# Kernel optimization log

Hardware: AMD Instinct MI355X
Metric: run time of the kernel (lower is better)

## Reference

```python
import jax, jax.numpy as jnp
import numpy as np

B, T, U = 8192, 1024, 1024  # batch, token_length, units

def _glorot(key, shape):
    fan_in, fan_out = shape
    limit = np.sqrt(6.0 / (fan_in + fan_out))
    return jax.random.uniform(key, shape, jnp.float32, -limit, limit)

def setup_inputs() -> dict:
    key = jax.random.key(0)
    ks = jax.random.split(key, 7)
    x = jax.random.normal(ks[0], (B, T), jnp.float32)
    h = jax.random.normal(ks[1], (B, U), jnp.float32)
    c = jax.random.normal(ks[2], (B, U), jnp.float32)
    W_i = _glorot(ks[3], (T + U, U))
    W_f = _glorot(ks[4], (T + U, U))
    W_g = _glorot(ks[5], (T + U, U))
    W_o = _glorot(ks[6], (T + U, U))
    b_i = jnp.zeros((U,), jnp.float32)
    b_f = jnp.zeros((U,), jnp.float32)
    b_g = jnp.zeros((U,), jnp.float32)
    b_o = jnp.zeros((U,), jnp.float32)
    return {"x": x, "h": h, "c": c, "W_i": W_i, "W_f": W_f, "W_g": W_g,
            "W_o": W_o, "b_i": b_i, "b_f": b_f, "b_g": b_g, "b_o": b_o}

def reference(x, h, c, W_i, W_f, W_g, W_o, b_i, b_f, b_g, b_o):
    x_h = jnp.concatenate([x, h], axis=-1)  # [B, T+U]
    # fused wide GEMM over the four gates
    W = jnp.concatenate([W_i, W_f, W_g, W_o], axis=1)  # [T+U, 4U]
    b = jnp.concatenate([b_i, b_f, b_g, b_o], axis=0)  # [4U]
    z = x_h @ W + b  # [B, 4U]
    zi, zf, zg, zo = jnp.split(z, 4, axis=-1)
    i = jax.nn.sigmoid(zi)
    f = jax.nn.sigmoid(zf)
    g = jnp.tanh(zg)
    o = jax.nn.sigmoid(zo)
    c_new = f * c + i * g
    h_new = o * jnp.tanh(c_new)
    return (h_new, c_new)
```

## Files before the change

### kernel.cpp

```cpp
#include <hip/hip_runtime.h>
#include <hip/hip_bf16.h>
#include <stdint.h>


typedef float f32x4 __attribute__((ext_vector_type(4)));
typedef __bf16 bf16x8 __attribute__((ext_vector_type(8)));

static __device__ __forceinline__ void gll16(const void* g, void* l) {
  __builtin_amdgcn_global_load_lds(
      (const __attribute__((address_space(1))) void*)g,
      (__attribute__((address_space(3))) void*)l, 16, 0, 0);
}

static __device__ __forceinline__ unsigned short f2bf(float f) {
  union { __hip_bfloat16 h; unsigned short u; } v{__float2bfloat16(f)};
  return v.u;
}

__global__ void pack_a(const float* __restrict__ x, const float* __restrict__ h,
                       char* __restrict__ Ap) {
  int row = blockIdx.x;
  int c8  = threadIdx.x;
  int kt  = c8 >> 2, kq = c8 & 3;
  int gk  = c8 * 8;
  const float* src = (gk < 1024) ? (x + (size_t)row * 1024 + gk)
                                 : (h + (size_t)row * 1024 + (gk - 1024));
  float4 lo = *(const float4*)src;
  float4 hi = *(const float4*)(src + 4);
  __attribute__((aligned(16))) unsigned short o[8] = {
      f2bf(lo.x), f2bf(lo.y), f2bf(lo.z), f2bf(lo.w),
      f2bf(hi.x), f2bf(hi.y), f2bf(hi.z), f2bf(hi.w) };
  int r = row & 255;
  int chunk = r * 4 + (kq ^ ((r >> 1) & 3));
  char* dst = Ap + ((size_t)((row >> 8) * 64 + kt)) * 16384 + chunk * 16;
  *(int4*)dst = *(const int4*)o;
}

__global__ void pack_w(const float* __restrict__ Wi, const float* __restrict__ Wf,
                       const float* __restrict__ Wg, const float* __restrict__ Wo,
                       char* __restrict__ Wp) {
  __shared__ float tile[32][65];
  int kt = blockIdx.x;
  int cbo = blockIdx.y;
  int g = blockIdx.z;
  const float* W = (g == 0) ? Wi : (g == 1) ? Wf : (g == 2) ? Wg : Wo;
  int t = threadIdx.x;
  {
    int k  = t >> 3;
    int c8 = (t & 7) * 8;
    const float* s = W + (size_t)(kt * 32 + k) * 1024 + cbo * 64 + c8;
    float4 lo = *(const float4*)s;
    float4 hi = *(const float4*)(s + 4);
    tile[k][c8 + 0] = lo.x; tile[k][c8 + 1] = lo.y; tile[k][c8 + 2] = lo.z; tile[k][c8 + 3] = lo.w;
    tile[k][c8 + 4] = hi.x; tile[k][c8 + 5] = hi.y; tile[k][c8 + 6] = hi.z; tile[k][c8 + 7] = hi.w;
  }
  __syncthreads();
  {
    int cl = t >> 2;
    int kq = t & 3;
    __attribute__((aligned(16))) unsigned short o[8];
#pragma unroll
    for (int j = 0; j < 8; ++j) o[j] = f2bf(tile[kq * 8 + j][cl]);
    int gc = ((cl >> 4) & 3) * 64 + g * 16 + (cl & 15);
    int chunk = gc * 4 + (kq ^ ((gc >> 1) & 3));
    char* dst = Wp + ((size_t)(cbo * 64 + kt)) * 16384 + chunk * 16;
    *(int4*)dst = *(const int4*)o;
  }
}

__global__ __launch_bounds__(512, 2)
void lstm_gemm(const char* __restrict__ Ap, const char* __restrict__ Wp,
               const float* __restrict__ c_in,
               const float* __restrict__ b_i, const float* __restrict__ b_f,
               const float* __restrict__ b_g, const float* __restrict__ b_o,
               float* __restrict__ out) {
  __shared__ __align__(128) char smem[131072];

  int tid = threadIdx.x;
  int w = tid >> 6, lane = tid & 63, l15 = lane & 15, lq = lane >> 4;
  int wm = w >> 2, wc = w & 3;

  int bid = blockIdx.x;
  int wg = (bid & 7) * 64 + (bid >> 3);
  int rbB = wg >> 4, cb = wg & 15;

  const char* aT = Ap + (size_t)rbB * (64 * 16384);
  const char* bT = Wp + (size_t)cb * (64 * 16384);

  f32x4 acc[8][4] = {};

  int aOff[8], bOff[4];
#pragma unroll
  for (int m = 0; m < 8; ++m) {
    int r = wm * 128 + m * 16 + l15;
    aOff[m] = r * 64 + ((lq ^ ((r >> 1) & 3)) << 4);
  }
#pragma unroll
  for (int n = 0; n < 4; ++n) {
    int gc = wc * 64 + n * 16 + l15;
    bOff[n] = gc * 64 + ((lq ^ ((gc >> 1) & 3)) << 4);
  }

  auto stgA = [&](int kt) {
    const char* s = aT + (size_t)kt * 16384 + tid * 16;
    char* d = smem + (kt & 3) * 32768 + tid * 16;
    gll16(s, d); gll16(s + 8192, d + 8192);
  };
  auto stgB = [&](int kt) {
    const char* s = bT + (size_t)kt * 16384 + tid * 16;
    char* d = smem + (kt & 3) * 32768 + 16384 + tid * 16;
    gll16(s, d); gll16(s + 8192, d + 8192);
  };

  stgA(0); stgB(0); stgA(1); stgB(1); stgA(2); stgB(2);
  asm volatile("s_waitcnt vmcnt(8)" ::: "memory");
  __builtin_amdgcn_s_barrier();

  for (int j = 0; j < 64; ++j) {
    const char* sA = smem + (j & 3) * 32768;
    const char* sB = sA + 16384;
    int js = (j + 3) & 63;

    bf16x8 aF[4], bF[4], aG[4];
#pragma unroll
    for (int m = 0; m < 4; ++m) aF[m] = *(const bf16x8*)(sA + aOff[m]);
#pragma unroll
    for (int n = 0; n < 4; ++n) bF[n] = *(const bf16x8*)(sB + bOff[n]);
    stgA(js);
    __builtin_amdgcn_s_barrier();
    __builtin_amdgcn_s_setprio(1);
#pragma unroll
    for (int m = 0; m < 4; ++m)
#pragma unroll
      for (int n = 0; n < 4; ++n)
        acc[m][n] = __builtin_amdgcn_mfma_f32_16x16x32_bf16(aF[m], bF[n], acc[m][n], 0, 0, 0);
    __builtin_amdgcn_s_setprio(0);
    __builtin_amdgcn_s_barrier();

#pragma unroll
    for (int m = 0; m < 4; ++m) aG[m] = *(const bf16x8*)(sA + aOff[4 + m]);
    stgB(js);
    __builtin_amdgcn_s_barrier();
    __builtin_amdgcn_s_setprio(1);
#pragma unroll
    for (int m = 0; m < 4; ++m)
#pragma unroll
      for (int n = 0; n < 4; ++n)
        acc[4 + m][n] = __builtin_amdgcn_mfma_f32_16x16x32_bf16(aG[m], bF[n], acc[4 + m][n], 0, 0, 0);
    __builtin_amdgcn_s_setprio(0);
    asm volatile("s_waitcnt vmcnt(8)" ::: "memory");
    __builtin_amdgcn_s_barrier();
  }

  int col = (cb * 4 + wc) * 16 + l15;
  float Bi = b_i[col], Bf = b_f[col], Bg = b_g[col], Bo = b_o[col];
  const size_t HN = (size_t)8192 * 1024;
#pragma unroll
  for (int mf = 0; mf < 8; ++mf) {
    int row0 = rbB * 256 + wm * 128 + mf * 16 + lq * 4;
#pragma unroll
    for (int r = 0; r < 4; ++r) {
      int row = row0 + r;
      float xi = acc[mf][0][r] + Bi, xf = acc[mf][1][r] + Bf;
      float xg = acc[mf][2][r] + Bg, xo = acc[mf][3][r] + Bo;
      float iv = 1.f / (1.f + __expf(-xi));
      float fv = 1.f / (1.f + __expf(-xf));
      float gv = 1.f - 2.f / (__expf(2.f * xg) + 1.f);
      float ov = 1.f / (1.f + __expf(-xo));
      float cv = c_in[(size_t)row * 1024 + col];
      float cn = fv * cv + iv * gv;
      float tc = 1.f - 2.f / (__expf(2.f * cn) + 1.f);
      out[(size_t)row * 1024 + col]      = ov * tc;
      out[HN + (size_t)row * 1024 + col] = cn;
    }
  }
}

extern "C" void kernel_launch(void* const* d_in, const int* in_sizes, int n_in,
                              void* d_out, int out_size, void* d_ws, size_t ws_size,
                              hipStream_t stream) {
  const float* x  = (const float*)d_in[0];
  const float* h  = (const float*)d_in[1];
  const float* c  = (const float*)d_in[2];
  const float* Wi = (const float*)d_in[3];
  const float* Wf = (const float*)d_in[4];
  const float* Wg = (const float*)d_in[5];
  const float* Wo = (const float*)d_in[6];
  const float* bi = (const float*)d_in[7];
  const float* bf = (const float*)d_in[8];
  const float* bg = (const float*)d_in[9];
  const float* bo = (const float*)d_in[10];

  char* Ap = (char*)d_ws;
  char* Wp = Ap + (size_t)8192 * 2048 * 2;
  float* out = (float*)d_out;

  hipLaunchKernelGGL(pack_a, dim3(8192), dim3(256), 0, stream, x, h, Ap);
  hipLaunchKernelGGL(pack_w, dim3(64, 16, 4), dim3(256), 0, stream, Wi, Wf, Wg, Wo, Wp);
  hipLaunchKernelGGL(lstm_gemm, dim3(512), dim3(512), 0, stream,
                     Ap, Wp, c, bi, bf, bg, bo, out);
}
```

Before: 313.3 us.

## Use K=64 tiles with double-buffered LDS and four-quadrant MFMA pipeline

Repacks A and W into 64-wide K tiles split into 128-row halves with an 8-way XOR swizzle. The GEMM main loop moves from 64 steps with 32-wide K and a 4-stage ring to 32 steps with 64-wide K and 2 LDS buffers. Each step is split into four MFMA quadrants interleaved with partial LDS reads and staggered global-to-LDS loads. The goal is fewer barriers per unit of work and finer overlap of loads with MFMA, at the cost of shallower prefetch and more complex wait accounting.

```diff
diff --git a/kernel.cpp b/kernel.cpp
--- a/kernel.cpp
+++ b/kernel.cpp
@@ -21,7 +21,7 @@
                        char* __restrict__ Ap) {
   int row = blockIdx.x;
   int c8  = threadIdx.x;
-  int kt  = c8 >> 2, kq = c8 & 3;
+  int kt  = c8 >> 3, q = c8 & 7;
   int gk  = c8 * 8;
   const float* src = (gk < 1024) ? (x + (size_t)row * 1024 + gk)
                                  : (h + (size_t)row * 1024 + (gk - 1024));
@@ -30,41 +30,48 @@
   __attribute__((aligned(16))) unsigned short o[8] = {
       f2bf(lo.x), f2bf(lo.y), f2bf(lo.z), f2bf(lo.w),
       f2bf(hi.x), f2bf(hi.y), f2bf(hi.z), f2bf(hi.w) };
-  int r = row & 255;
-  int chunk = r * 4 + (kq ^ ((r >> 1) & 3));
-  char* dst = Ap + ((size_t)((row >> 8) * 64 + kt)) * 16384 + chunk * 16;
-  *(int4*)dst = *(const int4*)o;
+  int rbB = row >> 8, half = (row >> 7) & 1, r = row & 127;
+  size_t dst = (((size_t)rbB * 32 + kt) * 2 + half) * 16384
+             + (size_t)(r * 8 + (q ^ (r & 7))) * 16;
+  *(int4*)(Ap + dst) = *(const int4*)o;
 }
 
 __global__ void pack_w(const float* __restrict__ Wi, const float* __restrict__ Wf,
                        const float* __restrict__ Wg, const float* __restrict__ Wo,
                        char* __restrict__ Wp) {
-  __shared__ float tile[32][65];
+  __shared__ float tile[64][65];
   int kt = blockIdx.x;
-  int cbo = blockIdx.y;
-  int g = blockIdx.z;
+  int cb = blockIdx.y;
+  int g  = blockIdx.z;
   const float* W = (g == 0) ? Wi : (g == 1) ? Wf : (g == 2) ? Wg : Wo;
   int t = threadIdx.x;
   {
-    int k  = t >> 3;
-    int c8 = (t & 7) * 8;
-    const float* s = W + (size_t)(kt * 32 + k) * 1024 + cbo * 64 + c8;
-    float4 lo = *(const float4*)s;
-    float4 hi = *(const float4*)(s + 4);
-    tile[k][c8 + 0] = lo.x; tile[k][c8 + 1] = lo.y; tile[k][c8 + 2] = lo.z; tile[k][c8 + 3] = lo.w;
-    tile[k][c8 + 4] = hi.x; tile[k][c8 + 5] = hi.y; tile[k][c8 + 6] = hi.z; tile[k][c8 + 7] = hi.w;
+    int k  = t >> 2;
+    int c8 = (t & 3) * 16;
+    const float* s = W + (size_t)(kt * 64 + k) * 1024 + cb * 64 + c8;
+#pragma unroll
+    for (int j4 = 0; j4 < 4; ++j4) {
+      float4 v = *(const float4*)(s + j4 * 4);
+      tile[k][c8 + j4 * 4 + 0] = v.x; tile[k][c8 + j4 * 4 + 1] = v.y;
+      tile[k][c8 + j4 * 4 + 2] = v.z; tile[k][c8 + j4 * 4 + 3] = v.w;
+    }
   }
   __syncthreads();
   {
     int cl = t >> 2;
     int kq = t & 3;
-    __attribute__((aligned(16))) unsigned short o[8];
-#pragma unroll
-    for (int j = 0; j < 8; ++j) o[j] = f2bf(tile[kq * 8 + j][cl]);
-    int gc = ((cl >> 4) & 3) * 64 + g * 16 + (cl & 15);
-    int chunk = gc * 4 + (kq ^ ((gc >> 1) & 3));
-    char* dst = Wp + ((size_t)(cbo * 64 + kt)) * 16384 + chunk * 16;
-    *(int4*)dst = *(const int4*)o;
+    int rloc = (cl >> 4) * 64 + g * 16 + (cl & 15);
+    int half = rloc >> 7, r = rloc & 127;
+#pragma unroll
+    for (int p = 0; p < 2; ++p) {
+      int q = kq + p * 4;
+      __attribute__((aligned(16))) unsigned short o[8];
+#pragma unroll
+      for (int j = 0; j < 8; ++j) o[j] = f2bf(tile[q * 8 + j][cl]);
+      size_t dst = (((size_t)cb * 32 + kt) * 2 + half) * 16384
+                 + (size_t)(r * 8 + (q ^ (r & 7))) * 16;
+      *(int4*)(Wp + dst) = *(const int4*)o;
+    }
   }
 }
 
@@ -84,73 +91,111 @@
   int wg = (bid & 7) * 64 + (bid >> 3);
   int rbB = wg >> 4, cb = wg & 15;
 
-  const char* aT = Ap + (size_t)rbB * (64 * 16384);
-  const char* bT = Wp + (size_t)cb * (64 * 16384);
+  const char* aT = Ap + (size_t)rbB * (32 * 2 * 16384);
+  const char* bT = Wp + (size_t)cb  * (32 * 2 * 16384);
 
   f32x4 acc[8][4] = {};
 
-  int aOff[8], bOff[4];
-#pragma unroll
-  for (int m = 0; m < 8; ++m) {
-    int r = wm * 128 + m * 16 + l15;
-    aOff[m] = r * 64 + ((lq ^ ((r >> 1) & 3)) << 4);
-  }
-#pragma unroll
-  for (int n = 0; n < 4; ++n) {
-    int gc = wc * 64 + n * 16 + l15;
-    bOff[n] = gc * 64 + ((lq ^ ((gc >> 1) & 3)) << 4);
-  }
-
-  auto stgA = [&](int kt) {
-    const char* s = aT + (size_t)kt * 16384 + tid * 16;
-    char* d = smem + (kt & 3) * 32768 + tid * 16;
-    gll16(s, d); gll16(s + 8192, d + 8192);
-  };
-  auto stgB = [&](int kt) {
-    const char* s = bT + (size_t)kt * 16384 + tid * 16;
-    char* d = smem + (kt & 3) * 32768 + 16384 + tid * 16;
-    gll16(s, d); gll16(s + 8192, d + 8192);
-  };
-
-  stgA(0); stgB(0); stgA(1); stgB(1); stgA(2); stgB(2);
-  asm volatile("s_waitcnt vmcnt(8)" ::: "memory");
-  __builtin_amdgcn_s_barrier();
-
-  for (int j = 0; j < 64; ++j) {
-    const char* sA = smem + (j & 3) * 32768;
-    const char* sB = sA + 16384;
-    int js = (j + 3) & 63;
-
-    bf16x8 aF[4], bF[4], aG[4];
-#pragma unroll
-    for (int m = 0; m < 4; ++m) aF[m] = *(const bf16x8*)(sA + aOff[m]);
-#pragma unroll
-    for (int n = 0; n < 4; ++n) bF[n] = *(const bf16x8*)(sB + bOff[n]);
-    stgA(js);
-    __builtin_amdgcn_s_barrier();
-    __builtin_amdgcn_s_setprio(1);
+  unsigned aOff[8][2], bOff[4][2];
+#pragma unroll
+  for (int mf = 0; mf < 8; ++mf) {
+    int r = mf * 16 + l15;
+#pragma unroll
+    for (int ks = 0; ks < 2; ++ks) {
+      int q = ks * 4 + lq;
+      aOff[mf][ks] = (unsigned)(wm * 16384 + (r * 8 + (q ^ (r & 7))) * 16);
+    }
+  }
+#pragma unroll
+  for (int nf = 0; nf < 4; ++nf) {
+    int r = (wc & 1) * 64 + nf * 16 + l15;
+#pragma unroll
+    for (int ks = 0; ks < 2; ++ks) {
+      int q = ks * 4 + lq;
+      bOff[nf][ks] = (unsigned)(32768 + (wc >> 1) * 16384 + (r * 8 + (q ^ (r & 7))) * 16);
+    }
+  }
+
+  auto stA = [&](int kt, int h) {
+    size_t s = (((size_t)(kt & 31)) * 2 + h) * 16384 + (size_t)tid * 16;
+    char* d = smem + (kt & 1) * 65536 + h * 16384 + tid * 16;
+    gll16(aT + s, d); gll16(aT + s + 8192, d + 8192);
+  };
+  auto stB = [&](int kt, int h) {
+    size_t s = (((size_t)(kt & 31)) * 2 + h) * 16384 + (size_t)tid * 16;
+    char* d = smem + (kt & 1) * 65536 + 32768 + h * 16384 + tid * 16;
+    gll16(bT + s, d); gll16(bT + s + 8192, d + 8192);
+  };
+
+#define BAR __builtin_amdgcn_s_barrier()
+#define PRIO1 __builtin_amdgcn_s_setprio(1)
+#define PRIO0 __builtin_amdgcn_s_setprio(0)
+#define VM6 asm volatile("s_waitcnt vmcnt(6)" ::: "memory")
+
+  stA(0, 0); stA(0, 1); stB(0, 0); stB(0, 1);
+  stB(1, 0); stA(1, 0); stB(1, 1);
+  VM6;
+  BAR;
+
+  bf16x8 aF[4][2], bN0[2][2], bN2[2][2];
+
+  auto LDA = [&](const char* s, int mb) {
 #pragma unroll
     for (int m = 0; m < 4; ++m)
 #pragma unroll
-      for (int n = 0; n < 4; ++n)
-        acc[m][n] = __builtin_amdgcn_mfma_f32_16x16x32_bf16(aF[m], bF[n], acc[m][n], 0, 0, 0);
-    __builtin_amdgcn_s_setprio(0);
-    __builtin_amdgcn_s_barrier();
-
-#pragma unroll
-    for (int m = 0; m < 4; ++m) aG[m] = *(const bf16x8*)(sA + aOff[4 + m]);
-    stgB(js);
-    __builtin_amdgcn_s_barrier();
-    __builtin_amdgcn_s_setprio(1);
+      for (int ks = 0; ks < 2; ++ks)
+        aF[m][ks] = *(const bf16x8*)(s + aOff[mb + m][ks]);
+  };
+  auto LDB = [&](const char* s, bf16x8 (&b)[2][2], int nb) {
+#pragma unroll
+    for (int n = 0; n < 2; ++n)
+#pragma unroll
+      for (int ks = 0; ks < 2; ++ks)
+        b[n][ks] = *(const bf16x8*)(s + bOff[nb + n][ks]);
+  };
+  auto Q = [&](int mb, int nb, bf16x8 (&b)[2][2]) {
 #pragma unroll
     for (int m = 0; m < 4; ++m)
 #pragma unroll
-      for (int n = 0; n < 4; ++n)
-        acc[4 + m][n] = __builtin_amdgcn_mfma_f32_16x16x32_bf16(aG[m], bF[n], acc[4 + m][n], 0, 0, 0);
-    __builtin_amdgcn_s_setprio(0);
-    asm volatile("s_waitcnt vmcnt(8)" ::: "memory");
-    __builtin_amdgcn_s_barrier();
-  }
+      for (int n = 0; n < 2; ++n)
+#pragma unroll
+        for (int ks = 0; ks < 2; ++ks)
+          acc[mb + m][nb + n] = __builtin_amdgcn_mfma_f32_16x16x32_bf16(
+              aF[m][ks], b[n][ks], acc[mb + m][nb + n], 0, 0, 0);
+  };
+
+  for (int it = 0; it < 16; ++it) {
+    int j = 2 * it;
+    const char* s0 = smem;
+    const char* s1 = smem + 65536;
+
+    LDA(s0, 0); LDB(s0, bN0, 0);
+    stA(j + 1, 1);
+    BAR; PRIO1; Q(0, 0, bN0); PRIO0; BAR;
+    LDB(s0, bN2, 2);
+    BAR; PRIO1; Q(0, 2, bN2); PRIO0; BAR;
+    LDA(s0, 4);
+    stB(j + 2, 0);
+    BAR; PRIO1; Q(4, 0, bN0); PRIO0; BAR;
+    stA(j + 2, 0); stB(j + 2, 1);
+    BAR; PRIO1; Q(4, 2, bN2); PRIO0;
+    VM6;
+    BAR;
+
+    LDA(s1, 0); LDB(s1, bN0, 0);
+    stA(j + 2, 1);
+    BAR; PRIO1; Q(0, 0, bN0); PRIO0; BAR;
+    LDB(s1, bN2, 2);
+    BAR; PRIO1; Q(0, 2, bN2); PRIO0; BAR;
+    LDA(s1, 4);
+    stB(j + 3, 0);
+    BAR; PRIO1; Q(4, 0, bN0); PRIO0; BAR;
+    stA(j + 3, 0); stB(j + 3, 1);
+    BAR; PRIO1; Q(4, 2, bN2); PRIO0;
+    VM6;
+    BAR;
+  }
+  asm volatile("s_waitcnt vmcnt(0)" ::: "memory");
 
   int col = (cb * 4 + wc) * 16 + l15;
   float Bi = b_i[col], Bf = b_f[col], Bg = b_g[col], Bo = b_o[col];
@@ -174,6 +219,10 @@
       out[HN + (size_t)row * 1024 + col] = cn;
     }
   }
+#undef BAR
+#undef PRIO1
+#undef PRIO0
+#undef VM6
 }
 
 extern "C" void kernel_launch(void* const* d_in, const int* in_sizes, int n_in,
@@ -196,7 +245,7 @@
   float* out = (float*)d_out;
 
   hipLaunchKernelGGL(pack_a, dim3(8192), dim3(256), 0, stream, x, h, Ap);
-  hipLaunchKernelGGL(pack_w, dim3(64, 16, 4), dim3(256), 0, stream, Wi, Wf, Wg, Wo, Wp);
+  hipLaunchKernelGGL(pack_w, dim3(32, 16, 4), dim3(256), 0, stream, Wi, Wf, Wg, Wo, Wp);
   hipLaunchKernelGGL(lstm_gemm, dim3(512), dim3(512), 0, stream,
                      Ap, Wp, c, bi, bf, bg, bo, out);
 }
```

After: 319.2 us. About the same (+1.9%).
